# Kernel optimization log

Hardware: AMD Instinct MI355X
Metric: run time of the kernel (lower is better)

Reference implementation:

```python
import jax, jax.numpy as jnp
import numpy as np

N_NODES = 20000  # number of atoms (scatter target count)


def setup_inputs() -> dict:
    key = jax.random.key(0)
    ks = jax.random.split(key, 7)
    E, F, R, L, O = 640000, 128, 16, 3, 12
    return {
        "m_ji": jax.random.normal(ks[0], (E, F), jnp.float32),
        "rbf_ji": jax.random.normal(ks[1], (E, R), jnp.float32),
        "atom_edge_index": jax.random.randint(ks[2], (2, E), 0, N_NODES, jnp.int64),
        "W_rbf": jax.random.normal(ks[3], (F, R), jnp.float32) * (1.0 / np.sqrt(R)),
        "dense_W": jax.random.normal(ks[4], (L, F, F), jnp.float32) * (1.0 / np.sqrt(F)),
        "dense_b": jax.random.normal(ks[5], (L, F), jnp.float32) * 0.01,
        "W_out": jax.random.normal(ks[6], (O, F), jnp.float32) * (1.0 / np.sqrt(F)),
    }


def reference(m_ji, rbf_ji, atom_edge_index, W_rbf, dense_W, dense_b, W_out):
    # e_ji = lin_rbf(rbf_ji): [E, dim_rbf] @ [dim_rbf, F] -> [E, F]
    e_ji = jnp.einsum("er,fr->ef", rbf_ji, W_rbf)
    # elementwise gate
    message_ji = e_ji * m_ji
    # scatter-add messages onto receiving atoms (index row 1)
    atom_i = jax.ops.segment_sum(message_ji, atom_edge_index[1], num_segments=N_NODES)
    # dense MLP stack with SiLU activation
    num_lin = dense_W.shape[0]
    for idx in range(num_lin):
        atom_i = jax.nn.silu(jnp.einsum("nf,gf->ng", atom_i, dense_W[idx]) + dense_b[idx])
    # final bias-free projection
    return jnp.einsum("nf,of->no", atom_i, W_out)
```

## Files before the change

kernel.cpp:

```cpp
#include <hip/hip_runtime.h>
#include <math.h>

#define F 128
#define R 16
#define O 12

__global__ void zero_int_kernel(int* __restrict__ p, int n) {
    int i = blockIdx.x * blockDim.x + threadIdx.x;
    if (i < n) p[i] = 0;
}

__global__ __launch_bounds__(256) void hist_kernel(
    const int* __restrict__ idx, int* __restrict__ cnt, int E)
{
    int i = blockIdx.x * blockDim.x + threadIdx.x;
    int stride = gridDim.x * blockDim.x;
    for (; i < E; i += stride) atomicAdd(&cnt[idx[i]], 1);
}

__global__ __launch_bounds__(1024) void scan_kernel(
    const int* __restrict__ cnt, int* __restrict__ off,
    int* __restrict__ cur, int N, int E)
{
    __shared__ int part[1024];
    int t = threadIdx.x;
    const int per = (N + 1023) / 1024;
    int s0 = t * per;
    int s = 0;
    for (int i = 0; i < per; i++) { int k = s0 + i; if (k < N) s += cnt[k]; }
    part[t] = s;
    __syncthreads();
    for (int d = 1; d < 1024; d <<= 1) {
        int v = (t >= d) ? part[t - d] : 0;
        __syncthreads();
        part[t] += v;
        __syncthreads();
    }
    int run = (t == 0) ? 0 : part[t - 1];
    for (int i = 0; i < per; i++) {
        int k = s0 + i;
        if (k < N) { off[k] = run; cur[k] = run; run += cnt[k]; }
    }
    if (t == 0) off[N] = E;
}

__global__ __launch_bounds__(256) void fill_kernel(
    const int* __restrict__ idx, int* __restrict__ cur,
    int* __restrict__ csr, int E)
{
    int i = blockIdx.x * blockDim.x + threadIdx.x;
    int stride = gridDim.x * blockDim.x;
    for (; i < E; i += stride) {
        int n = idx[i];
        int p = atomicAdd(&cur[n], 1);
        csr[p] = i;
    }
}

__global__ __launch_bounds__(256) void gather_kernel(
    const float* __restrict__ m, const float* __restrict__ rbf,
    const int* __restrict__ csr, const int* __restrict__ off,
    const float* __restrict__ Wrbf, float* __restrict__ A, int N)
{
    int lane = threadIdx.x & 63;
    int w = threadIdx.x >> 6;
    int n = blockIdx.x * 4 + w;
    if (n >= N) return;

    int f0 = lane << 1;
    float4 W0[4], W1[4];
    #pragma unroll
    for (int q = 0; q < 4; q++) {
        W0[q] = *(const float4*)(Wrbf + (size_t)f0 * R + q * 4);
        W1[q] = *(const float4*)(Wrbf + (size_t)(f0 + 1) * R + q * 4);
    }

    float a0 = 0.f, a1 = 0.f;
    int jb = off[n], je = off[n + 1];

    int j = jb;
    for (; j + 1 < je; j += 2) {
        int e0 = csr[j], e1 = csr[j + 1];
        const float4* rpa = (const float4*)(rbf + (size_t)e0 * R);
        const float4* rpb = (const float4*)(rbf + (size_t)e1 * R);
        float4 p0 = rpa[0], p1 = rpa[1], p2 = rpa[2], p3 = rpa[3];
        float4 q0 = rpb[0], q1 = rpb[1], q2 = rpb[2], q3 = rpb[3];
        float2 ma = *(const float2*)(m + (size_t)e0 * F + f0);
        float2 mb = *(const float2*)(m + (size_t)e1 * F + f0);

        float d0a = p0.x*W0[0].x + p0.y*W0[0].y + p0.z*W0[0].z + p0.w*W0[0].w
                  + p1.x*W0[1].x + p1.y*W0[1].y + p1.z*W0[1].z + p1.w*W0[1].w
                  + p2.x*W0[2].x + p2.y*W0[2].y + p2.z*W0[2].z + p2.w*W0[2].w
                  + p3.x*W0[3].x + p3.y*W0[3].y + p3.z*W0[3].z + p3.w*W0[3].w;
        float d1a = p0.x*W1[0].x + p0.y*W1[0].y + p0.z*W1[0].z + p0.w*W1[0].w
                  + p1.x*W1[1].x + p1.y*W1[1].y + p1.z*W1[1].z + p1.w*W1[1].w
                  + p2.x*W1[2].x + p2.y*W1[2].y + p2.z*W1[2].z + p2.w*W1[2].w
                  + p3.x*W1[3].x + p3.y*W1[3].y + p3.z*W1[3].z + p3.w*W1[3].w;
        float d0b = q0.x*W0[0].x + q0.y*W0[0].y + q0.z*W0[0].z + q0.w*W0[0].w
                  + q1.x*W0[1].x + q1.y*W0[1].y + q1.z*W0[1].z + q1.w*W0[1].w
                  + q2.x*W0[2].x + q2.y*W0[2].y + q2.z*W0[2].z + q2.w*W0[2].w
                  + q3.x*W0[3].x + q3.y*W0[3].y + q3.z*W0[3].z + q3.w*W0[3].w;
        float d1b = q0.x*W1[0].x + q0.y*W1[0].y + q0.z*W1[0].z + q0.w*W1[0].w
                  + q1.x*W1[1].x + q1.y*W1[1].y + q1.z*W1[1].z + q1.w*W1[1].w
                  + q2.x*W1[2].x + q2.y*W1[2].y + q2.z*W1[2].z + q2.w*W1[2].w
                  + q3.x*W1[3].x + q3.y*W1[3].y + q3.z*W1[3].z + q3.w*W1[3].w;

        a0 += d0a * ma.x + d0b * mb.x;
        a1 += d1a * ma.y + d1b * mb.y;
    }
    if (j < je) {
        int e0 = csr[j];
        const float4* rpa = (const float4*)(rbf + (size_t)e0 * R);
        float4 p0 = rpa[0], p1 = rpa[1], p2 = rpa[2], p3 = rpa[3];
        float2 ma = *(const float2*)(m + (size_t)e0 * F + f0);
        float d0a = p0.x*W0[0].x + p0.y*W0[0].y + p0.z*W0[0].z + p0.w*W0[0].w
                  + p1.x*W0[1].x + p1.y*W0[1].y + p1.z*W0[1].z + p1.w*W0[1].w
                  + p2.x*W0[2].x + p2.y*W0[2].y + p2.z*W0[2].z + p2.w*W0[2].w
                  + p3.x*W0[3].x + p3.y*W0[3].y + p3.z*W0[3].z + p3.w*W0[3].w;
        float d1a = p0.x*W1[0].x + p0.y*W1[0].y + p0.z*W1[0].z + p0.w*W1[0].w
                  + p1.x*W1[1].x + p1.y*W1[1].y + p1.z*W1[1].z + p1.w*W1[1].w
                  + p2.x*W1[2].x + p2.y*W1[2].y + p2.z*W1[2].z + p2.w*W1[2].w
                  + p3.x*W1[3].x + p3.y*W1[3].y + p3.z*W1[3].z + p3.w*W1[3].w;
        a0 += d0a * ma.x;
        a1 += d1a * ma.y;
    }

    *(float2*)(A + (size_t)n * F + f0) = make_float2(a0, a1);
}

__global__ __launch_bounds__(256) void mlp_layer(
    const float* __restrict__ in, const float* __restrict__ W,
    const float* __restrict__ b, float* __restrict__ out, int N)
{
    __shared__ float Ws[F * F];
    int t = threadIdx.x;
    int base = blockIdx.x * 64;

    for (int s = t; s < F * F / 4; s += 256) {
        int g = s >> 5, c = s & 31;
        float4 v = *(const float4*)(W + g * F + (c << 2));
        *(float4*)(Ws + g * F + ((c ^ (g & 31)) << 2)) = v;
    }
    __syncthreads();

    int j = t & 15, i = t >> 4;
    float acc[4][8];
    #pragma unroll
    for (int k = 0; k < 4; k++)
        #pragma unroll
        for (int mm = 0; mm < 8; mm++) acc[k][mm] = 0.f;

    int  n0[4]; bool ok[4];
    #pragma unroll
    for (int k = 0; k < 4; k++) { n0[k] = base + i + 16 * k; ok[k] = n0[k] < N; }

    for (int c = 0; c < 32; c++) {
        int f = c << 2;
        float4 av[4];
        #pragma unroll
        for (int k = 0; k < 4; k++)
            av[k] = ok[k] ? *(const float4*)(in + (size_t)n0[k] * F + f)
                          : make_float4(0.f, 0.f, 0.f, 0.f);
        float4 wv[8];
        #pragma unroll
        for (int mm = 0; mm < 8; mm++) {
            int g = j + 16 * mm;
            wv[mm] = *(const float4*)(Ws + g * F + ((c ^ (g & 31)) << 2));
        }
        #pragma unroll
        for (int k = 0; k < 4; k++)
            #pragma unroll
            for (int mm = 0; mm < 8; mm++)
                acc[k][mm] += av[k].x * wv[mm].x + av[k].y * wv[mm].y +
                              av[k].z * wv[mm].z + av[k].w * wv[mm].w;
    }

    #pragma unroll
    for (int mm = 0; mm < 8; mm++) {
        int g = j + 16 * mm;
        float bias = b[g];
        #pragma unroll
        for (int k = 0; k < 4; k++) if (ok[k]) {
            float x = acc[k][mm] + bias;
            float y = x / (1.f + __expf(-x));
            out[(size_t)n0[k] * F + g] = y;
        }
    }
}

__global__ __launch_bounds__(256) void proj_kernel(
    const float* __restrict__ act, const float* __restrict__ Wout,
    float* __restrict__ out, int N)
{
    __shared__ float Ws[O * F];
    int t = threadIdx.x;
    for (int s = t; s < O * F; s += 256) Ws[s] = Wout[s];
    __syncthreads();

    int w = t >> 6, lane = t & 63;
    int n = blockIdx.x * 4 + w;
    if (n >= N) return;

    float a0 = act[(size_t)n * F + lane];
    float a1 = act[(size_t)n * F + 64 + lane];
    #pragma unroll
    for (int o = 0; o < O; o++) {
        float p = a0 * Ws[o * F + lane] + a1 * Ws[o * F + 64 + lane];
        #pragma unroll
        for (int off = 32; off >= 1; off >>= 1) p += __shfl_xor(p, off, 64);
        if (lane == 0) out[n * O + o] = p;
    }
}

extern "C" void kernel_launch(void* const* d_in, const int* in_sizes, int n_in,
                              void* d_out, int out_size, void* d_ws, size_t ws_size,
                              hipStream_t stream)
{
    const float* m    = (const float*)d_in[0];
    const float* rbf  = (const float*)d_in[1];
    const int*   aei  = (const int*)d_in[2];
    const float* Wrbf = (const float*)d_in[3];
    const float* dW   = (const float*)d_in[4];
    const float* db   = (const float*)d_in[5];
    const float* Wout = (const float*)d_in[6];
    float* out = (float*)d_out;

    int E = in_sizes[0] / F;
    int N = out_size / O;

    float* A = (float*)d_ws;
    float* B = A + (size_t)N * F;
    int* csr = (int*)B;
    int* cnt = csr + E;
    int* cur = cnt + N;
    int* off = cur + N;

    const int* idx1 = aei + E;

    zero_int_kernel<<<(N + 255) / 256, 256, 0, stream>>>(cnt, N);
    hist_kernel<<<1024, 256, 0, stream>>>(idx1, cnt, E);
    scan_kernel<<<1, 1024, 0, stream>>>(cnt, off, cur, N, E);
    fill_kernel<<<1024, 256, 0, stream>>>(idx1, cur, csr, E);
    gather_kernel<<<(N + 3) / 4, 256, 0, stream>>>(m, rbf, csr, off, Wrbf, A, N);

    int mb = (N + 63) / 64;
    mlp_layer<<<mb, 256, 0, stream>>>(A, dW + 0 * F * F, db + 0 * F, B, N);
    mlp_layer<<<mb, 256, 0, stream>>>(B, dW + 1 * F * F, db + 1 * F, A, N);
    mlp_layer<<<mb, 256, 0, stream>>>(A, dW + 2 * F * F, db + 2 * F, B, N);

    proj_kernel<<<(N + 3) / 4, 256, 0, stream>>>(B, Wout, out, N);
}
```

Measured before the change: 818.6 us.

## Fuse MLP layers and projection into one kernel; batch CSR index loads via shuffles

```diff
diff --git a/kernel.cpp b/kernel.cpp
--- a/kernel.cpp
+++ b/kernel.cpp
@@ -4,6 +4,7 @@
 #define F 128
 #define R 16
 #define O 12
+#define NB 32
 
 __global__ void zero_int_kernel(int* __restrict__ p, int n) {
     int i = blockIdx.x * blockDim.x + threadIdx.x;
@@ -57,6 +58,14 @@
     }
 }
 
+__device__ __forceinline__ float dot16(const float4* r, const float4* Wv) {
+    float s = 0.f;
+    #pragma unroll
+    for (int q = 0; q < 4; q++)
+        s += r[q].x * Wv[q].x + r[q].y * Wv[q].y + r[q].z * Wv[q].z + r[q].w * Wv[q].w;
+    return s;
+}
+
 __global__ __launch_bounds__(256) void gather_kernel(
     const float* __restrict__ m, const float* __restrict__ rbf,
     const int* __restrict__ csr, const int* __restrict__ off,
@@ -78,137 +87,135 @@
     float a0 = 0.f, a1 = 0.f;
     int jb = off[n], je = off[n + 1];
 
-    int j = jb;
-    for (; j + 1 < je; j += 2) {
-        int e0 = csr[j], e1 = csr[j + 1];
-        const float4* rpa = (const float4*)(rbf + (size_t)e0 * R);
-        const float4* rpb = (const float4*)(rbf + (size_t)e1 * R);
-        float4 p0 = rpa[0], p1 = rpa[1], p2 = rpa[2], p3 = rpa[3];
-        float4 q0 = rpb[0], q1 = rpb[1], q2 = rpb[2], q3 = rpb[3];
-        float2 ma = *(const float2*)(m + (size_t)e0 * F + f0);
-        float2 mb = *(const float2*)(m + (size_t)e1 * F + f0);
-
-        float d0a = p0.x*W0[0].x + p0.y*W0[0].y + p0.z*W0[0].z + p0.w*W0[0].w
-                  + p1.x*W0[1].x + p1.y*W0[1].y + p1.z*W0[1].z + p1.w*W0[1].w
-                  + p2.x*W0[2].x + p2.y*W0[2].y + p2.z*W0[2].z + p2.w*W0[2].w
-                  + p3.x*W0[3].x + p3.y*W0[3].y + p3.z*W0[3].z + p3.w*W0[3].w;
-        float d1a = p0.x*W1[0].x + p0.y*W1[0].y + p0.z*W1[0].z + p0.w*W1[0].w
-                  + p1.x*W1[1].x + p1.y*W1[1].y + p1.z*W1[1].z + p1.w*W1[1].w
-                  + p2.x*W1[2].x + p2.y*W1[2].y + p2.z*W1[2].z + p2.w*W1[2].w
-                  + p3.x*W1[3].x + p3.y*W1[3].y + p3.z*W1[3].z + p3.w*W1[3].w;
-        float d0b = q0.x*W0[0].x + q0.y*W0[0].y + q0.z*W0[0].z + q0.w*W0[0].w
-                  + q1.x*W0[1].x + q1.y*W0[1].y + q1.z*W0[1].z + q1.w*W0[1].w
-                  + q2.x*W0[2].x + q2.y*W0[2].y + q2.z*W0[2].z + q2.w*W0[2].w
-                  + q3.x*W0[3].x + q3.y*W0[3].y + q3.z*W0[3].z + q3.w*W0[3].w;
-        float d1b = q0.x*W1[0].x + q0.y*W1[0].y + q0.z*W1[0].z + q0.w*W1[0].w
-                  + q1.x*W1[1].x + q1.y*W1[1].y + q1.z*W1[1].z + q1.w*W1[1].w
-                  + q2.x*W1[2].x + q2.y*W1[2].y + q2.z*W1[2].z + q2.w*W1[2].w
-                  + q3.x*W1[3].x + q3.y*W1[3].y + q3.z*W1[3].z + q3.w*W1[3].w;
-
-        a0 += d0a * ma.x + d0b * mb.x;
-        a1 += d1a * ma.y + d1b * mb.y;
-    }
-    if (j < je) {
-        int e0 = csr[j];
-        const float4* rpa = (const float4*)(rbf + (size_t)e0 * R);
-        float4 p0 = rpa[0], p1 = rpa[1], p2 = rpa[2], p3 = rpa[3];
-        float2 ma = *(const float2*)(m + (size_t)e0 * F + f0);
-        float d0a = p0.x*W0[0].x + p0.y*W0[0].y + p0.z*W0[0].z + p0.w*W0[0].w
-                  + p1.x*W0[1].x + p1.y*W0[1].y + p1.z*W0[1].z + p1.w*W0[1].w
-                  + p2.x*W0[2].x + p2.y*W0[2].y + p2.z*W0[2].z + p2.w*W0[2].w
-                  + p3.x*W0[3].x + p3.y*W0[3].y + p3.z*W0[3].z + p3.w*W0[3].w;
-        float d1a = p0.x*W1[0].x + p0.y*W1[0].y + p0.z*W1[0].z + p0.w*W1[0].w
-                  + p1.x*W1[1].x + p1.y*W1[1].y + p1.z*W1[1].z + p1.w*W1[1].w
-                  + p2.x*W1[2].x + p2.y*W1[2].y + p2.z*W1[2].z + p2.w*W1[2].w
-                  + p3.x*W1[3].x + p3.y*W1[3].y + p3.z*W1[3].z + p3.w*W1[3].w;
-        a0 += d0a * ma.x;
-        a1 += d1a * ma.y;
+    for (int base = jb; base < je; base += 64) {
+        int cnt = min(64, je - base);
+        int ec = (base + lane < je) ? csr[base + lane] : 0;
+        int jj = 0;
+        for (; jj + 4 <= cnt; jj += 4) {
+            int e0 = __shfl(ec, jj);
+            int e1 = __shfl(ec, jj + 1);
+            int e2 = __shfl(ec, jj + 2);
+            int e3 = __shfl(ec, jj + 3);
+            float2 m0 = *(const float2*)(m + (size_t)e0 * F + f0);
+            float2 m1 = *(const float2*)(m + (size_t)e1 * F + f0);
+            float2 m2 = *(const float2*)(m + (size_t)e2 * F + f0);
+            float2 m3 = *(const float2*)(m + (size_t)e3 * F + f0);
+            float4 r0[4], r1[4], r2[4], r3[4];
+            #pragma unroll
+            for (int q = 0; q < 4; q++) {
+                r0[q] = ((const float4*)(rbf + (size_t)e0 * R))[q];
+                r1[q] = ((const float4*)(rbf + (size_t)e1 * R))[q];
+                r2[q] = ((const float4*)(rbf + (size_t)e2 * R))[q];
+                r3[q] = ((const float4*)(rbf + (size_t)e3 * R))[q];
+            }
+            a0 += dot16(r0, W0) * m0.x;  a1 += dot16(r0, W1) * m0.y;
+            a0 += dot16(r1, W0) * m1.x;  a1 += dot16(r1, W1) * m1.y;
+            a0 += dot16(r2, W0) * m2.x;  a1 += dot16(r2, W1) * m2.y;
+            a0 += dot16(r3, W0) * m3.x;  a1 += dot16(r3, W1) * m3.y;
+        }
+        for (; jj < cnt; jj++) {
+            int e0 = __shfl(ec, jj);
+            float2 m0 = *(const float2*)(m + (size_t)e0 * F + f0);
+            float4 r0[4];
+            #pragma unroll
+            for (int q = 0; q < 4; q++)
+                r0[q] = ((const float4*)(rbf + (size_t)e0 * R))[q];
+            a0 += dot16(r0, W0) * m0.x;
+            a1 += dot16(r0, W1) * m0.y;
+        }
     }
 
     *(float2*)(A + (size_t)n * F + f0) = make_float2(a0, a1);
 }
 
-__global__ __launch_bounds__(256) void mlp_layer(
-    const float* __restrict__ in, const float* __restrict__ W,
-    const float* __restrict__ b, float* __restrict__ out, int N)
+__global__ __launch_bounds__(256) void mlp_fused(
+    const float* __restrict__ A, const float* __restrict__ dW,
+    const float* __restrict__ db, const float* __restrict__ Wout,
+    float* __restrict__ out, int N)
 {
     __shared__ float Ws[F * F];
+    __shared__ float act[NB * F];
     int t = threadIdx.x;
-    int base = blockIdx.x * 64;
-
-    for (int s = t; s < F * F / 4; s += 256) {
-        int g = s >> 5, c = s & 31;
-        float4 v = *(const float4*)(W + g * F + (c << 2));
-        *(float4*)(Ws + g * F + ((c ^ (g & 31)) << 2)) = v;
-    }
-    __syncthreads();
-
+    int base = blockIdx.x * NB;
     int j = t & 15, i = t >> 4;
-    float acc[4][8];
+
+    int  n0[2]; bool ok[2];
     #pragma unroll
-    for (int k = 0; k < 4; k++)
+    for (int k = 0; k < 2; k++) { n0[k] = base + i + 16 * k; ok[k] = n0[k] < N; }
+
+    for (int l = 0; l < 3; l++) {
+        __syncthreads();
+        for (int s = t; s < F * F / 4; s += 256) {
+            int g = s >> 5, c = s & 31;
+            float4 v = *(const float4*)(dW + (size_t)l * F * F + g * F + (c << 2));
+            *(float4*)(Ws + g * F + ((c ^ (g & 31)) << 2)) = v;
+        }
+        __syncthreads();
+
+        float acc[2][8];
         #pragma unroll
-        for (int mm = 0; mm < 8; mm++) acc[k][mm] = 0.f;
-
-    int  n0[4]; bool ok[4];
-    #pragma unroll
-    for (int k = 0; k < 4; k++) { n0[k] = base + i + 16 * k; ok[k] = n0[k] < N; }
-
-    for (int c = 0; c < 32; c++) {
-        int f = c << 2;
-        float4 av[4];
-        #pragma unroll
-        for (int k = 0; k < 4; k++)
-            av[k] = ok[k] ? *(const float4*)(in + (size_t)n0[k] * F + f)
-                          : make_float4(0.f, 0.f, 0.f, 0.f);
-        float4 wv[8];
+        for (int k = 0; k < 2; k++)
+            #pragma unroll
+            for (int mm = 0; mm < 8; mm++) acc[k][mm] = 0.f;
+
+        for (int c = 0; c < 32; c++) {
+            int f = c << 2;
+            float4 av[2];
+            #pragma unroll
+            for (int k = 0; k < 2; k++) {
+                if (l == 0)
+                    av[k] = ok[k] ? *(const float4*)(A + (size_t)n0[k] * F + f)
+                                  : make_float4(0.f, 0.f, 0.f, 0.f);
+                else
+                    av[k] = *(const float4*)(act + (i + 16 * k) * F + f);
+            }
+            float4 wv[8];
+            #pragma unroll
+            for (int mm = 0; mm < 8; mm++) {
+                int g = j + 16 * mm;
+                wv[mm] = *(const float4*)(Ws + g * F + ((c ^ (g & 31)) << 2));
+            }
+            #pragma unroll
+            for (int k = 0; k < 2; k++)
+                #pragma unroll
+                for (int mm = 0; mm < 8; mm++)
+                    acc[k][mm] += av[k].x * wv[mm].x + av[k].y * wv[mm].y +
+                                  av[k].z * wv[mm].z + av[k].w * wv[mm].w;
+        }
+
         #pragma unroll
         for (int mm = 0; mm < 8; mm++) {
             int g = j + 16 * mm;
-            wv[mm] = *(const float4*)(Ws + g * F + ((c ^ (g & 31)) << 2));
-        }
-        #pragma unroll
-        for (int k = 0; k < 4; k++)
-            #pragma unroll
-            for (int mm = 0; mm < 8; mm++)
-                acc[k][mm] += av[k].x * wv[mm].x + av[k].y * wv[mm].y +
-                              av[k].z * wv[mm].z + av[k].w * wv[mm].w;
-    }
-
-    #pragma unroll
-    for (int mm = 0; mm < 8; mm++) {
-        int g = j + 16 * mm;
-        float bias = b[g];
-        #pragma unroll
-        for (int k = 0; k < 4; k++) if (ok[k]) {
-            float x = acc[k][mm] + bias;
-            float y = x / (1.f + __expf(-x));
-            out[(size_t)n0[k] * F + g] = y;
-        }
-    }
-}
-
-__global__ __launch_bounds__(256) void proj_kernel(
-    const float* __restrict__ act, const float* __restrict__ Wout,
-    float* __restrict__ out, int N)
-{
-    __shared__ float Ws[O * F];
-    int t = threadIdx.x;
-    for (int s = t; s < O * F; s += 256) Ws[s] = Wout[s];
+            float bias = db[l * F + g];
+            #pragma unroll
+            for (int k = 0; k < 2; k++) {
+                float x = acc[k][mm] + bias;
+                act[(i + 16 * k) * F + g] = x / (1.f + __expf(-x));
+            }
+        }
+    }
+
     __syncthreads();
-
-    int w = t >> 6, lane = t & 63;
-    int n = blockIdx.x * 4 + w;
-    if (n >= N) return;
-
-    float a0 = act[(size_t)n * F + lane];
-    float a1 = act[(size_t)n * F + 64 + lane];
-    #pragma unroll
-    for (int o = 0; o < O; o++) {
-        float p = a0 * Ws[o * F + lane] + a1 * Ws[o * F + 64 + lane];
-        #pragma unroll
-        for (int off = 32; off >= 1; off >>= 1) p += __shfl_xor(p, off, 64);
-        if (lane == 0) out[n * O + o] = p;
+    for (int s = t; s < O * F / 4; s += 256)
+        ((float4*)Ws)[s] = ((const float4*)Wout)[s];
+    __syncthreads();
+
+    int nl = t >> 3;
+    int oq = t & 7;
+    int n = base + nl;
+    if (n < N) {
+        float s0 = 0.f, s1 = 0.f;
+        for (int f = 0; f < F; f += 4) {
+            float4 a  = *(const float4*)(act + nl * F + f);
+            float4 w0 = *(const float4*)(Ws + oq * F + f);
+            s0 += a.x * w0.x + a.y * w0.y + a.z * w0.z + a.w * w0.w;
+            if (oq < 4) {
+                float4 w1 = *(const float4*)(Ws + (8 + oq) * F + f);
+                s1 += a.x * w1.x + a.y * w1.y + a.z * w1.z + a.w * w1.w;
+            }
+        }
+        out[(size_t)n * O + oq] = s0;
+        if (oq < 4) out[(size_t)n * O + 8 + oq] = s1;
     }
 }
 
@@ -229,8 +236,7 @@
     int N = out_size / O;
 
     float* A = (float*)d_ws;
-    float* B = A + (size_t)N * F;
-    int* csr = (int*)B;
+    int* csr = (int*)(A + (size_t)N * F);
     int* cnt = csr + E;
     int* cur = cnt + N;
     int* off = cur + N;
@@ -243,10 +249,5 @@
     fill_kernel<<<1024, 256, 0, stream>>>(idx1, cur, csr, E);
     gather_kernel<<<(N + 3) / 4, 256, 0, stream>>>(m, rbf, csr, off, Wrbf, A, N);
 
-    int mb = (N + 63) / 64;
-    mlp_layer<<<mb, 256, 0, stream>>>(A, dW + 0 * F * F, db + 0 * F, B, N);
-    mlp_layer<<<mb, 256, 0, stream>>>(B, dW + 1 * F * F, db + 1 * F, A, N);
-    mlp_layer<<<mb, 256, 0, stream>>>(A, dW + 2 * F * F, db + 2 * F, B, N);
-
-    proj_kernel<<<(N + 3) / 4, 256, 0, stream>>>(B, Wout, out, N);
-}
+    mlp_fused<<<(N + NB - 1) / NB, 256, 0, stream>>>(A, dW, db, Wout, out, N);
+}
```

Measured after the change: 903.8 us. 10.4% more time.
